# Performance work log

Measured on AMD Instinct MI355X. Metric: run time of the kernel, lower is better.

Reference implementation:

```python
import jax, jax.numpy as jnp
import numpy as np

EPS = 1e-5  # torch InstanceNorm1d default eps


def _instance_norm(x, gamma, beta):
    # per-sample, per-channel stats over the length dim; biased variance (torch semantics)
    mu = jnp.mean(x, axis=-1, keepdims=True)
    var = jnp.var(x, axis=-1, keepdims=True)
    return (x - mu) / jnp.sqrt(var + EPS) * gamma[None, :, None] + beta[None, :, None]


def _forward(x_ft, gamma, beta):
    # x_ft: complex [B, C, N]
    N = x_ft.shape[-1]
    x = jnp.real(jnp.fft.ifft(x_ft, norm='forward'))  # [B, C, N] real
    # The torch loop runs res = base_res .. N, each iteration overwriting the
    # low/high frequency bands of x_out in-place. The final iteration
    # (res == N) writes EVERY entry of x_out (the two band slices cover all
    # N//2+1 rfft bins), so the module's output -- and its gradients, since
    # overwritten writes carry zero cotangent -- equal the res == N
    # computation alone. resample_1d(x, N) copies the full spectrum and is a
    # spectral identity, so x_res == x.
    xr = _instance_norm(x, gamma, beta)
    xr = jax.nn.gelu(xr, approximate=False)  # exact GELU, matches torch nn.GELU
    # Faithful to the source: inside the loop torch.fft.rfft2 is used, i.e. a
    # 2D transform over the last two dims (channel, length).
    x_out = jnp.fft.rfft2(xr, norm='forward')  # complex [B, C, N//2 + 1]
    out = jnp.fft.fft(jnp.fft.irfft(x_out, n=N, norm='forward'), norm='forward')
    return out  # complex [B, C, N]


def setup_inputs() -> dict:
    key = jax.random.key(0)
    k1, k2 = jax.random.split(key)
    B, C, N = 16, 128, 8192
    return {
        'x_ft_real': jax.random.normal(k1, (B, C, N), dtype=jnp.float32),
        'x_ft_imag': jax.random.normal(k2, (B, C, N), dtype=jnp.float32),
        'gamma': jnp.ones((C,), dtype=jnp.float32),
        'beta': jnp.zeros((C,), dtype=jnp.float32),
    }


def reference(x_ft_real, x_ft_imag, gamma, beta):
    out = _forward(jax.lax.complex(x_ft_real, x_ft_imag), gamma, beta)
    # return real/imag parts as separate float arrays (harness-friendly)
    return (jnp.real(out), jnp.imag(out))
```

## Files before the change

### kernel.cpp

```cpp
#include <hip/hip_runtime.h>
#include <math.h>

static constexpr int kN = 8192;
static constexpr int kC = 128;
static constexpr int kB = 16;
static constexpr float kScale = 0.5f / 1048576.0f;

#define C8  0.70710678118654752f
#define CP8 0.92387953251128676f
#define SP8 0.38268343236508977f

typedef float v2f __attribute__((ext_vector_type(2)));

__device__ __forceinline__ v2f mk2(float x, float y){ v2f r; r.x=x; r.y=y; return r; }
__device__ __forceinline__ v2f imul(v2f a){ return mk2(-a.y, a.x); }
__device__ __forceinline__ v2f mimul(v2f a){ return mk2(a.y, -a.x); }
__device__ __forceinline__ v2f cconj(v2f a){ return mk2(a.x, -a.y); }
__device__ __forceinline__ v2f cmul(v2f a, v2f b){
    return mk2(a.x*b.x - a.y*b.y, a.x*b.y + a.y*b.x);
}

__device__ __forceinline__ v2f wrev(float rev){
    return mk2(__builtin_amdgcn_cosf(rev), __builtin_amdgcn_sinf(rev));
}

__device__ __forceinline__ int swz(int n){ return n ^ ((n>>4)&15); }

#define REV(k) ((((k)&3)<<2)|((k)>>2))

template<int SGN>
__device__ __forceinline__ void dft4(v2f&a, v2f&b, v2f&c, v2f&d){
    v2f t0=a+c, t1=a-c, t2=b+d, t3=b-d;
    v2f j3 = (SGN>0) ? imul(t3) : mimul(t3);
    a = t0+t2; b = t1+j3; c = t0-t2; d = t1-j3;
}

template<int SGN>
__device__ __forceinline__ void dft16(v2f* v){
    dft4<SGN>(v[0], v[4], v[8],  v[12]);
    dft4<SGN>(v[1], v[5], v[9],  v[13]);
    dft4<SGN>(v[2], v[6], v[10], v[14]);
    dft4<SGN>(v[3], v[7], v[11], v[15]);
    const float sg = (SGN>0)? 1.f : -1.f;
    const v2f W1 = mk2(CP8,  sg*SP8);
    const v2f W2 = mk2(C8,   sg*C8);
    const v2f W3 = mk2(SP8,  sg*CP8);
    const v2f W6 = mk2(-C8,  sg*C8);
    const v2f W9 = mk2(-CP8, -sg*SP8);
    v[5]  = cmul(v[5],  W1);
    v[9]  = cmul(v[9],  W2);
    v[13] = cmul(v[13], W3);
    v[6]  = cmul(v[6],  W2);
    v[10] = (SGN>0)? imul(v[10]) : mimul(v[10]);
    v[14] = cmul(v[14], W6);
    v[7]  = cmul(v[7],  W3);
    v[11] = cmul(v[11], W6);
    v[15] = cmul(v[15], W9);
    dft4<SGN>(v[0],  v[1],  v[2],  v[3]);
    dft4<SGN>(v[4],  v[5],  v[6],  v[7]);
    dft4<SGN>(v[8],  v[9],  v[10], v[11]);
    dft4<SGN>(v[12], v[13], v[14], v[15]);
}

__device__ __forceinline__ void twid_dif(v2f* v, v2f w1){
    v2f w2=cmul(w1,w1), w3=cmul(w2,w1), w4=cmul(w2,w2);
    v2f w5=cmul(w2,w3), w6=cmul(w3,w3), w7=cmul(w3,w4), w8=cmul(w4,w4);
    v2f w9=cmul(w4,w5), w10=cmul(w5,w5), w11=cmul(w5,w6), w12=cmul(w6,w6);
    v2f w13=cmul(w6,w7), w14=cmul(w7,w7), w15=cmul(w7,w8);
    v[4] =cmul(v[4], w1);  v[8] =cmul(v[8], w2);  v[12]=cmul(v[12],w3);
    v[1] =cmul(v[1], w4);  v[5] =cmul(v[5], w5);  v[9] =cmul(v[9], w6);
    v[13]=cmul(v[13],w7);  v[2] =cmul(v[2], w8);  v[6] =cmul(v[6], w9);
    v[10]=cmul(v[10],w10); v[14]=cmul(v[14],w11); v[3] =cmul(v[3], w12);
    v[7] =cmul(v[7], w13); v[11]=cmul(v[11],w14); v[15]=cmul(v[15],w15);
}
__device__ __forceinline__ void twid_dit(v2f* v, v2f w1){
    v2f w2=cmul(w1,w1), w3=cmul(w2,w1), w4=cmul(w2,w2);
    v2f w5=cmul(w2,w3), w6=cmul(w3,w3), w7=cmul(w3,w4), w8=cmul(w4,w4);
    v2f w9=cmul(w4,w5), w10=cmul(w5,w5), w11=cmul(w5,w6), w12=cmul(w6,w6);
    v2f w13=cmul(w6,w7), w14=cmul(w7,w7), w15=cmul(w7,w8);
    v[1] =cmul(v[1], w1);  v[2] =cmul(v[2], w2);  v[3] =cmul(v[3], w3);
    v[4] =cmul(v[4], w4);  v[5] =cmul(v[5], w5);  v[6] =cmul(v[6], w6);
    v[7] =cmul(v[7], w7);  v[8] =cmul(v[8], w8);  v[9] =cmul(v[9], w9);
    v[10]=cmul(v[10],w10); v[11]=cmul(v[11],w11); v[12]=cmul(v[12],w12);
    v[13]=cmul(v[13],w13); v[14]=cmul(v[14],w14); v[15]=cmul(v[15],w15);
}

__device__ __forceinline__ v2f gelu2(v2f v){
    v2f z = v * (0.7978845608028654f + 0.0356774081363001f * v * v);
    float e0 = __builtin_amdgcn_exp2f(-2.8853900817779268f * z.x);
    float e1 = __builtin_amdgcn_exp2f(-2.8853900817779268f * z.y);
    return mk2(v.x / (1.0f + e0), v.y / (1.0f + e1));
}

__global__ __launch_bounds__(256, 4) void k1_row(
    const float* __restrict__ xr, const float* __restrict__ xi,
    const float* __restrict__ gamma, const float* __restrict__ beta,
    float* __restrict__ outR, float* __restrict__ outI)
{
    __shared__ v2f buf[4096];
    __shared__ v2f Twb[16];
    __shared__ float sred[4];

    const int p   = threadIdx.x;
    const int row = blockIdx.x;
    const int ch  = row & (kC-1);

    if (p < 16) Twb[p] = wrev((float)p * (1.0f/256.0f));
    const int i0 = ((p>>4)<<8) + (p&15);

    v2f v[16];

    const float* rR = xr + (size_t)row * kN;
    const float* rI = xi + (size_t)row * kN;

    const float mean = 2.0f * rR[0];

    float pq = 0.f;
    #pragma unroll
    for (int j = 0; j < 16; ++j) {
        int k   = p + (j<<8);
        int km  = (kN - k) & (kN-1);
        int km2 = 4096 - k;
        v2f w = wrev((float)k * (1.0f/8192.0f));
        v2f Hk  = mk2(rR[k]+rR[km],       rI[k]-rI[km]);
        v2f Hk2 = mk2(rR[k+4096]+rR[km2], rI[k+4096]-rI[km2]);
        pq += Hk.x*Hk.x + Hk.y*Hk.y + Hk2.x*Hk2.x + Hk2.y*Hk2.y;
        v2f S = Hk + Hk2, D = Hk - Hk2;
        v2f P = cmul(D, w);
        v[j] = S + imul(P);
    }
    #pragma unroll
    for (int off = 32; off >= 1; off >>= 1)
        pq += __shfl_down(pq, off);
    if ((p & 63) == 0) sred[p>>6] = pq;

    dft16<1>(v);
    twid_dif(v, wrev((float)p * (1.0f/4096.0f)));
    #pragma unroll
    for (int m = 0; m < 16; ++m) buf[swz(p + (m<<8))] = v[REV(m)];
    __syncthreads();

    float total = sred[0] + sred[1] + sred[2] + sred[3];
    float var  = total - mean*mean;
    float gg = gamma[ch] * rsqrtf(var + 1e-5f);
    float bb = beta[ch] - mean * gg;

    const v2f wB = Twb[p & 15];
    #pragma unroll
    for (int j = 0; j < 16; ++j) v[j] = buf[swz(i0 + (j<<4))];
    dft16<1>(v);
    twid_dif(v, wB);
    #pragma unroll
    for (int m = 0; m < 16; ++m) buf[swz(i0 + (m<<4))] = v[REV(m)];
    __builtin_amdgcn_wave_barrier();

    #pragma unroll
    for (int j = 0; j < 16; ++j) v[j] = buf[swz((p<<4) + j)];
    dft16<1>(v);

    #pragma unroll
    for (int j = 0; j < 16; ++j) v[j] = gelu2(v[j] * gg + bb);

    {
        v2f u[16];
        #pragma unroll
        for (int j = 0; j < 16; ++j) u[j] = v[REV(j)];
        dft16<-1>(u);
        #pragma unroll
        for (int m = 0; m < 16; ++m) buf[swz((p<<4) + m)] = u[REV(m)];
    }
    __builtin_amdgcn_wave_barrier();

    #pragma unroll
    for (int j = 0; j < 16; ++j) v[j] = buf[swz(i0 + (j<<4))];
    twid_dit(v, cconj(wB));
    dft16<-1>(v);
    #pragma unroll
    for (int m = 0; m < 16; ++m) buf[swz(i0 + (m<<4))] = v[REV(m)];
    __syncthreads();

    #pragma unroll
    for (int j = 0; j < 16; ++j) v[j] = buf[swz(p + (j<<8))];
    twid_dit(v, cconj(wrev((float)p * (1.0f/4096.0f))));
    dft16<-1>(v);
    float* oR = outR + (size_t)row * kN;
    float* oI = outI + (size_t)row * kN;
    #pragma unroll
    for (int m = 0; m < 16; ++m) {
        int k = p + (m<<8);
        oR[k] = v[REV(m)].x;
        oI[k] = v[REV(m)].y;
    }
}

__global__ __launch_bounds__(256, 2) void k2_col(float* __restrict__ outR,
                                                 float* __restrict__ outI)
{
    __shared__ v2f tile[kC][32];
    __shared__ v2f tw[64];

    const int tid  = threadIdx.x;
    const int j    = tid & 31;
    const int g    = tid >> 5;
    const int b    = blockIdx.y;
    const int k0   = blockIdx.x << 5;
    const int colA = k0 + j;
    const bool valid = (colA <= 2048);
    const int colB = (4096 - colA) & 4095;

    if (tid < 64) {
        tw[tid] = mk2(__builtin_amdgcn_cosf((float)tid * (1.0f/128.0f)),
                      -__builtin_amdgcn_sinf((float)tid * (1.0f/128.0f)));
    }
    const float wc =  __builtin_amdgcn_cosf((float)colA * (1.0f/8192.0f));
    const float ws = -__builtin_amdgcn_sinf((float)colA * (1.0f/8192.0f));

    float* baseR = outR + (size_t)b * kC * kN;
    float* baseI = outI + (size_t)b * kC * kN;

    v2f yb[16];
    #pragma unroll
    for (int ci = 0; ci < 16; ++ci) {
        const int c = g + (ci << 3);
        v2f YA = mk2(0.f, 0.f), YB = mk2(0.f, 0.f);
        if (valid) {
            size_t offA = (size_t)c * kN + colA;
            size_t offB = (size_t)c * kN + colB;
            float Zx  = baseR[offA], Zy  = baseI[offA];
            float Zmx = baseR[offB], Zmy = baseI[offB];
            float Sx = Zx + Zmx, Sy = Zy - Zmy;
            float Dx = Zx - Zmx, Dy = Zy + Zmy;
            float Px = Dx*wc - Dy*ws, Py = Dx*ws + Dy*wc;
            YA = mk2(Sx + Py,  Sy - Px);
            YB = mk2(Sx - Py, -Sy - Px);
        }
        tile[c][j] = YA;
        yb[ci] = YB;
    }
    __syncthreads();

    for (int st = 7; st >= 1; --st) {
        const int h = 1 << (st-1);
        #pragma unroll
        for (int s = 0; s < 8; ++s) {
            int q   = g + (s<<3);
            int pos = q & (h-1);
            int i0  = ((q >> (st-1)) << st) + pos;
            int i1  = i0 + h;
            v2f a = tile[i0][j], bb = tile[i1][j];
            v2f w = tw[pos << (7-st)];
            tile[i0][j] = a + bb;
            tile[i1][j] = cmul(a - bb, w);
        }
        __syncthreads();
    }
    if (valid) {
        for (int p = g; p < kC; p += 8) {
            int f = (int)(__brev((unsigned)p) >> 25);
            v2f vv = tile[p][j] * kScale;
            size_t off = (size_t)f * kN + colA;
            if (colA == 0) {
                baseR[off] = vv.x; baseI[off] = 0.f;
            } else {
                baseR[off] = vv.x; baseI[off] = vv.y;
                size_t offm = (size_t)f * kN + (kN - colA);
                baseR[offm] = vv.x; baseI[offm] = -vv.y;
            }
        }
    }
    __syncthreads();

    #pragma unroll
    for (int ci = 0; ci < 16; ++ci) {
        const int c = g + (ci << 3);
        tile[c][j] = yb[ci];
    }
    __syncthreads();

    for (int st = 7; st >= 1; --st) {
        const int h = 1 << (st-1);
        #pragma unroll
        for (int s = 0; s < 8; ++s) {
            int q   = g + (s<<3);
            int pos = q & (h-1);
            int i0  = ((q >> (st-1)) << st) + pos;
            int i1  = i0 + h;
            v2f a = tile[i0][j], bb = tile[i1][j];
            v2f w = tw[pos << (7-st)];
            tile[i0][j] = a + bb;
            tile[i1][j] = cmul(a - bb, w);
        }
        __syncthreads();
    }
    if (valid) {
        const int kkB = 4096 - colA;
        for (int p = g; p < kC; p += 8) {
            int f = (int)(__brev((unsigned)p) >> 25);
            v2f vv = tile[p][j] * kScale;
            size_t off = (size_t)f * kN + kkB;
            if (kkB == 4096) {
                baseR[off] = vv.x; baseI[off] = 0.f;
            } else {
                baseR[off] = vv.x; baseI[off] = vv.y;
                size_t offm = (size_t)f * kN + (kN - kkB);
                baseR[offm] = vv.x; baseI[offm] = -vv.y;
            }
        }
    }
}

extern "C" void kernel_launch(void* const* d_in, const int* in_sizes, int n_in,
                              void* d_out, int out_size, void* d_ws, size_t ws_size,
                              hipStream_t stream)
{
    const float* xr    = (const float*)d_in[0];
    const float* xi    = (const float*)d_in[1];
    const float* gamma = (const float*)d_in[2];
    const float* beta  = (const float*)d_in[3];

    float* outR = (float*)d_out;
    float* outI = outR + (size_t)kB * kC * kN;

    k1_row<<<kB * kC, 256, 0, stream>>>(xr, xi, gamma, beta, outR, outI);
    k2_col<<<dim3(65, kB), 256, 0, stream>>>(outR, outI);
}
```

Baseline: 107.8 us.

## Remap block indices for XCD locality, add setprio, precompute row twiddles

Block indices in both kernels are remapped so that consecutive blocks (round-robined across the 8 XCDs) map to distinct batches. Blocks on the same XCD then share a batch, which is meant to improve L2 locality between the row and column kernels. The per-element twiddle computation in the first pass becomes one transcendental per thread times a compile-time constant table, which drops 15 sin/cos pairs per thread at a small cost in accuracy. s_setprio raises wave priority around the FFT compute sections, to favour compute-phase waves over memory-phase ones.

After: 119.9 us. +11.2%, slower.

```diff
diff --git a/kernel.cpp b/kernel.cpp
--- a/kernel.cpp
+++ b/kernel.cpp
@@ -92,6 +92,23 @@
     return mk2(v.x / (1.0f + e0), v.y / (1.0f + e1));
 }
 
+#define WJ(j) ( (j)==0 ? mk2(1.f,0.f) : \
+  (j)==1  ? mk2( 0.98078528f, 0.19509032f) : \
+  (j)==2  ? mk2( 0.92387953f, 0.38268343f) : \
+  (j)==3  ? mk2( 0.83146961f, 0.55557023f) : \
+  (j)==4  ? mk2( 0.70710678f, 0.70710678f) : \
+  (j)==5  ? mk2( 0.55557023f, 0.83146961f) : \
+  (j)==6  ? mk2( 0.38268343f, 0.92387953f) : \
+  (j)==7  ? mk2( 0.19509032f, 0.98078528f) : \
+  (j)==8  ? mk2( 0.f,         1.f        ) : \
+  (j)==9  ? mk2(-0.19509032f, 0.98078528f) : \
+  (j)==10 ? mk2(-0.38268343f, 0.92387953f) : \
+  (j)==11 ? mk2(-0.55557023f, 0.83146961f) : \
+  (j)==12 ? mk2(-0.70710678f, 0.70710678f) : \
+  (j)==13 ? mk2(-0.83146961f, 0.55557023f) : \
+  (j)==14 ? mk2(-0.92387953f, 0.38268343f) : \
+            mk2(-0.98078528f, 0.19509032f) )
+
 __global__ __launch_bounds__(256, 4) void k1_row(
     const float* __restrict__ xr, const float* __restrict__ xi,
     const float* __restrict__ gamma, const float* __restrict__ beta,
@@ -101,9 +118,12 @@
     __shared__ v2f Twb[16];
     __shared__ float sred[4];
 
-    const int p   = threadIdx.x;
-    const int row = blockIdx.x;
-    const int ch  = row & (kC-1);
+    const int p    = threadIdx.x;
+    const int bx   = blockIdx.x;
+    const int rest = bx >> 3;
+    const int bch  = (bx & 7) | ((rest >> 7) << 3);
+    const int ch   = rest & 127;
+    const int row  = (bch << 7) | ch;
 
     if (p < 16) Twb[p] = wrev((float)p * (1.0f/256.0f));
     const int i0 = ((p>>4)<<8) + (p&15);
@@ -115,13 +135,14 @@
 
     const float mean = 2.0f * rR[0];
 
+    const v2f wp = wrev((float)p * (1.0f/8192.0f));
     float pq = 0.f;
     #pragma unroll
     for (int j = 0; j < 16; ++j) {
         int k   = p + (j<<8);
         int km  = (kN - k) & (kN-1);
         int km2 = 4096 - k;
-        v2f w = wrev((float)k * (1.0f/8192.0f));
+        v2f w = cmul(wp, WJ(j));
         v2f Hk  = mk2(rR[k]+rR[km],       rI[k]-rI[km]);
         v2f Hk2 = mk2(rR[k+4096]+rR[km2], rI[k+4096]-rI[km2]);
         pq += Hk.x*Hk.x + Hk.y*Hk.y + Hk2.x*Hk2.x + Hk2.y*Hk2.y;
@@ -134,8 +155,10 @@
         pq += __shfl_down(pq, off);
     if ((p & 63) == 0) sred[p>>6] = pq;
 
+    __builtin_amdgcn_s_setprio(1);
     dft16<1>(v);
     twid_dif(v, wrev((float)p * (1.0f/4096.0f)));
+    __builtin_amdgcn_s_setprio(0);
     #pragma unroll
     for (int m = 0; m < 16; ++m) buf[swz(p + (m<<8))] = v[REV(m)];
     __syncthreads();
@@ -148,24 +171,26 @@
     const v2f wB = Twb[p & 15];
     #pragma unroll
     for (int j = 0; j < 16; ++j) v[j] = buf[swz(i0 + (j<<4))];
+    __builtin_amdgcn_s_setprio(1);
     dft16<1>(v);
     twid_dif(v, wB);
+    __builtin_amdgcn_s_setprio(0);
     #pragma unroll
     for (int m = 0; m < 16; ++m) buf[swz(i0 + (m<<4))] = v[REV(m)];
     __builtin_amdgcn_wave_barrier();
 
     #pragma unroll
     for (int j = 0; j < 16; ++j) v[j] = buf[swz((p<<4) + j)];
+    __builtin_amdgcn_s_setprio(1);
     dft16<1>(v);
-
     #pragma unroll
     for (int j = 0; j < 16; ++j) v[j] = gelu2(v[j] * gg + bb);
-
     {
         v2f u[16];
         #pragma unroll
         for (int j = 0; j < 16; ++j) u[j] = v[REV(j)];
         dft16<-1>(u);
+        __builtin_amdgcn_s_setprio(0);
         #pragma unroll
         for (int m = 0; m < 16; ++m) buf[swz((p<<4) + m)] = u[REV(m)];
     }
@@ -173,16 +198,20 @@
 
     #pragma unroll
     for (int j = 0; j < 16; ++j) v[j] = buf[swz(i0 + (j<<4))];
+    __builtin_amdgcn_s_setprio(1);
     twid_dit(v, cconj(wB));
     dft16<-1>(v);
+    __builtin_amdgcn_s_setprio(0);
     #pragma unroll
     for (int m = 0; m < 16; ++m) buf[swz(i0 + (m<<4))] = v[REV(m)];
     __syncthreads();
 
     #pragma unroll
     for (int j = 0; j < 16; ++j) v[j] = buf[swz(p + (j<<8))];
+    __builtin_amdgcn_s_setprio(1);
     twid_dit(v, cconj(wrev((float)p * (1.0f/4096.0f))));
     dft16<-1>(v);
+    __builtin_amdgcn_s_setprio(0);
     float* oR = outR + (size_t)row * kN;
     float* oI = outI + (size_t)row * kN;
     #pragma unroll
@@ -202,8 +231,9 @@
     const int tid  = threadIdx.x;
     const int j    = tid & 31;
     const int g    = tid >> 5;
-    const int b    = blockIdx.y;
-    const int k0   = blockIdx.x << 5;
+    const int gx   = blockIdx.x;
+    const int b    = (gx & 7) | (blockIdx.y << 3);
+    const int k0   = (gx >> 3) << 5;
     const int colA = k0 + j;
     const bool valid = (colA <= 2048);
     const int colB = (4096 - colA) & 4095;
@@ -322,5 +352,5 @@
     float* outI = outR + (size_t)kB * kC * kN;
 
     k1_row<<<kB * kC, 256, 0, stream>>>(xr, xi, gamma, beta, outR, outI);
-    k2_col<<<dim3(65, kB), 256, 0, stream>>>(outR, outI);
-}
+    k2_col<<<dim3(520, 2), 256, 0, stream>>>(outR, outI);
+}
```
